# Performance work log

Hardware: AMD Instinct MI355X
Metric: run time of the kernel (lower is better)

## Reference

```python
import jax, jax.numpy as jnp
import numpy as np

K, d = 8, 8
D = K * d          # 64
B, T, N = 8, 12, 325


def _xavier(key, shape):
    fan_out, fan_in = shape
    lim = (6.0 / (fan_in + fan_out)) ** 0.5
    return jax.random.uniform(key, shape, jnp.float32, -lim, lim)


def setup_inputs() -> dict:
    key = jax.random.key(0)
    ks = jax.random.split(key, 8)
    return {
        "X": jax.random.normal(ks[0], (B, T, N, D), jnp.float32),
        "STE": jax.random.normal(ks[1], (B, T, N, D), jnp.float32),
        "adj": jax.random.randint(ks[2], (N, N), 0, 2, jnp.int32),
        "W7": _xavier(ks[3], (D, 2 * D)), "b7": jnp.zeros((D,), jnp.float32),
        "W8": _xavier(ks[4], (D, 2 * D)), "b8": jnp.zeros((D,), jnp.float32),
        "W9": _xavier(ks[5], (D, 2 * D)), "b9": jnp.zeros((D,), jnp.float32),
        "W10": _xavier(ks[6], (D, D)), "b10": jnp.zeros((D,), jnp.float32),
        "W11": _xavier(ks[7], (D, D)), "b11": jnp.zeros((D,), jnp.float32),
    }


def reference(X, STE, adj, W7, b7, W8, b8, W9, b9, W10, b10, W11, b11):
    # X, STE: [B, T, N, D]
    x = jnp.concatenate([X, STE], axis=-1)  # [B,T,N,2D]
    gelu = lambda t: jax.nn.gelu(t, approximate=False)  # torch F.gelu default = exact erf
    q = gelu(x @ W7.T + b7)  # [B,T,N,D]
    k = gelu(x @ W8.T + b8)
    v = gelu(x @ W9.T + b9)
    # split D into K heads of size d (equivalent to torch split(dim=-1)+cat(dim=0))
    heads = lambda t: t.reshape(B, T, N, K, d)
    q, k, v = heads(q), heads(k), heads(v)
    # scores: [K,B,T,N,N] == torch's [K*B,T,N,N]
    attn = jnp.einsum('btnkd,btmkd->kbtnm', q, k) / (d ** 0.5)
    attn = jnp.where(adj > 0, attn, jnp.float32(-9e15))
    attn = jax.nn.softmax(attn, axis=-1)
    out = jnp.einsum('kbtnm,btmkd->btnkd', attn, v).reshape(B, T, N, D)
    out = gelu(out @ W10.T + b10) @ W11.T + b11
    return out
```

## Files before the change

### kernel.cpp

```cpp
#include <hip/hip_runtime.h>
#include <math.h>

#define NN 325
#define BT 96
#define NROWS (BT * NN)
#define SCL (0.35355339059327373f * 1.4426950408889634f)

typedef _Float16 half_t;
typedef half_t half4_t __attribute__((ext_vector_type(4)));
typedef half_t half2_t __attribute__((ext_vector_type(2)));
typedef float float4_t __attribute__((ext_vector_type(4)));

__device__ __forceinline__ float gelu_f(float x) {
    return 0.5f * x * (1.0f + erff(x * 0.70710678118654752f));
}

__global__ void prep_kernel(const int* __restrict__ adj,
                            const float* __restrict__ W7,
                            const float* __restrict__ W8,
                            const float* __restrict__ W9,
                            const float* __restrict__ W10,
                            const float* __restrict__ W11,
                            unsigned int* __restrict__ packedT,
                            half_t* __restrict__ w789,
                            half_t* __restrict__ wab)
{
    int idx = blockIdx.x * 256 + threadIdx.x;
    if (idx < 11 * NN) {
        int w = idx / NN, n = idx - w * NN;
        unsigned int bits = 0u;
        #pragma unroll 8
        for (int j = 0; j < 32; ++j) {
            int m = w * 32 + j;
            if (m < NN && adj[n * NN + m] > 0) bits |= (1u << j);
        }
        packedT[w * NN + n] = bits;
    } else if (idx < 3575 + 24576) {
        int i = idx - 3575;
        int p = i >> 13, r = i & 8191;
        const float* Wp = (p == 0) ? W7 : (p == 1) ? W8 : W9;
        w789[i] = (half_t)Wp[r];
    } else if (idx < 3575 + 24576 + 8192) {
        int i = idx - 28151;
        int p = i >> 12, r = i & 4095;
        wab[i] = (half_t)(p ? W11[r] : W10[r]);
    }
}

#define XS 136

__device__ __forceinline__ void qkv_stage_w(const half_t* __restrict__ src,
                                            half_t* dst, int tid)
{
    #pragma unroll
    for (int idx = tid; idx < 1024; idx += 512) {
        int c = idx >> 4, g = idx & 15;
        *(uint4*)&dst[c * XS + g * 8] = *(const uint4*)&src[c * 128 + g * 8];
    }
}

__device__ __forceinline__ void qkv_compute(
    const half_t* x16, const half_t* wb, const float* __restrict__ b,
    half_t* __restrict__ outp, float oscale,
    int row0, int rbase, int ch, int l15, int quad)
{
    float4_t acc[2];
    #pragma unroll
    for (int cc = 0; cc < 2; ++cc) {
        float bias = b[(ch * 2 + cc) * 16 + l15];
        acc[cc] = (float4_t){bias, bias, bias, bias};
    }
    #pragma unroll
    for (int kk = 0; kk < 8; ++kk) {
        half4_t a = *(const half4_t*)&x16[(rbase + l15) * XS + kk * 16 + quad * 4];
        #pragma unroll
        for (int cc = 0; cc < 2; ++cc) {
            half4_t bf = *(const half4_t*)
                &wb[((ch * 2 + cc) * 16 + l15) * XS + kk * 16 + quad * 4];
            acc[cc] = __builtin_amdgcn_mfma_f32_16x16x16f16(a, bf, acc[cc], 0, 0, 0);
        }
    }
    #pragma unroll
    for (int cc = 0; cc < 2; ++cc) {
        #pragma unroll
        for (int rr = 0; rr < 4; ++rr) {
            int R = row0 + rbase + quad * 4 + rr;
            if (R < NROWS)
                outp[R * 64 + (ch * 2 + cc) * 16 + l15] =
                    (half_t)(gelu_f(acc[cc][rr]) * oscale);
        }
    }
}

__global__ __launch_bounds__(512) void qkv_kernel(
    const float* __restrict__ X, const float* __restrict__ STE,
    const half_t* __restrict__ w789,
    const float* __restrict__ b7, const float* __restrict__ b8,
    const float* __restrict__ b9,
    half_t* __restrict__ q, half_t* __restrict__ k, half_t* __restrict__ v)
{
    __shared__ __attribute__((aligned(16))) half_t x16[64 * XS];
    __shared__ __attribute__((aligned(16))) half_t wbuf[2][64 * XS];
    const int tid  = threadIdx.x;
    const int row0 = blockIdx.x * 64;

    #pragma unroll
    for (int idx = tid; idx < 2048; idx += 512) {
        int r = idx >> 5, c4 = idx & 31;
        int R = row0 + r;
        float4 f = {0.f, 0.f, 0.f, 0.f};
        if (R < NROWS)
            f = (c4 < 16) ? *(const float4*)(X + R * 64 + c4 * 4)
                          : *(const float4*)(STE + R * 64 + (c4 - 16) * 4);
        half4_t hv;
        hv[0] = (half_t)f.x; hv[1] = (half_t)f.y;
        hv[2] = (half_t)f.z; hv[3] = (half_t)f.w;
        *(half4_t*)&x16[r * XS + c4 * 4] = hv;
    }
    qkv_stage_w(w789, wbuf[0], tid);
    __syncthreads();

    const int lane = tid & 63, wv = tid >> 6;
    const int l15 = lane & 15, quad = lane >> 4;
    const int rbase = (wv & 3) * 16, ch = wv >> 2;

    qkv_stage_w(w789 + 8192, wbuf[1], tid);
    qkv_compute(x16, wbuf[0], b7, q, SCL, row0, rbase, ch, l15, quad);
    __syncthreads();

    qkv_stage_w(w789 + 16384, wbuf[0], tid);
    qkv_compute(x16, wbuf[1], b8, k, 1.0f, row0, rbase, ch, l15, quad);
    __syncthreads();

    qkv_compute(x16, wbuf[0], b9, v, 1.0f, row0, rbase, ch, l15, quad);
}

__global__ __launch_bounds__(256) void attn_kernel(
    const half_t* __restrict__ q16g, const half_t* __restrict__ k16g,
    const half_t* __restrict__ v16g, const unsigned int* __restrict__ packedT,
    half_t* __restrict__ ao)
{
    __shared__ __attribute__((aligned(16))) half_t K16[336 * 20];
    __shared__ __attribute__((aligned(16))) half_t VT16[16 * 344];
    const int tid = threadIdx.x;
    const int h = blockIdx.x, bt = blockIdx.y;
    const long base = (long)(bt * NN) * 64 + h * 8;

    const half4_t z4 = {(half_t)0.f, (half_t)0.f, (half_t)0.f, (half_t)0.f};

    for (int idx = tid; idx < 16 * 344 / 2; idx += 256)
        ((half2_t*)VT16)[idx] = (half2_t)(half_t)0.f;
    __syncthreads();
    for (int i = tid; i < 344; i += 256)
        VT16[8 * 344 + i] = (half_t)1.0f;

    for (int r = tid; r < 336; r += 256) {
        half4_t ka = z4, kb = z4;
        if (r < NN) {
            ka = *(const half4_t*)(k16g + base + r * 64);
            kb = *(const half4_t*)(k16g + base + r * 64 + 4);
        }
        *(half4_t*)&K16[r * 20]      = ka;
        *(half4_t*)&K16[r * 20 + 4]  = kb;
        *(half4_t*)&K16[r * 20 + 8]  = z4;
        *(half4_t*)&K16[r * 20 + 12] = z4;
    }

    for (int mp = tid; mp < 168; mp += 256) {
        int m0 = 2 * mp, m1 = 2 * mp + 1;
        half4_t v0a = z4, v0b = z4, v1a = z4, v1b = z4;
        if (m0 < NN) {
            v0a = *(const half4_t*)(v16g + base + m0 * 64);
            v0b = *(const half4_t*)(v16g + base + m0 * 64 + 4);
        }
        if (m1 < NN) {
            v1a = *(const half4_t*)(v16g + base + m1 * 64);
            v1b = *(const half4_t*)(v16g + base + m1 * 64 + 4);
        }
        #pragma unroll
        for (int c = 0; c < 4; ++c) {
            half2_t p0; p0[0] = v0a[c]; p0[1] = v1a[c];
            half2_t p1; p1[0] = v0b[c]; p1[1] = v1b[c];
            *(half2_t*)&VT16[c * 344 + 2 * mp]       = p0;
            *(half2_t*)&VT16[(c + 4) * 344 + 2 * mp] = p1;
        }
    }
    __syncthreads();

    const int lane = tid & 63;
    const int wv   = tid >> 6;
    const int l15  = lane & 15;
    const int quad = lane >> 4;
    const int qsh  = quad * 4;

    for (int t = wv; t < 21; t += 4) {
        const int n  = t * 16 + l15;
        const int nq = (n < NN) ? n : (NN - 1);

        half4_t qf = z4;
        if (quad < 2)
            qf = *(const half4_t*)(q16g + base + (long)nq * 64 + qsh);

        float rm = 0.0f;
        #pragma unroll
        for (int mt = 0; mt < 21; ++mt) {
            half4_t kf = *(const half4_t*)&K16[(mt * 16 + l15) * 20 + qsh];
            float4_t s = __builtin_amdgcn_mfma_f32_16x16x16f16(
                kf, qf, (float4_t){0.f, 0.f, 0.f, 0.f}, 0, 0, 0);
            rm = fmaxf(rm, fmaxf(fmaxf(s[0], s[1]), fmaxf(s[2], s[3])));
        }
        rm = fmaxf(rm, __shfl_xor(rm, 16, 64));
        rm = fmaxf(rm, __shfl_xor(rm, 32, 64));

        unsigned int mb[11];
        #pragma unroll
        for (int w = 0; w < 11; ++w) mb[w] = packedT[w * NN + nq];

        const float4_t cinit = {-rm, -rm, -rm, -rm};
        float4_t acc = {0.f, 0.f, 0.f, 0.f};
        #pragma unroll
        for (int mt = 0; mt < 21; ++mt) {
            half4_t kf = *(const half4_t*)&K16[(mt * 16 + l15) * 20 + qsh];
            float4_t s = __builtin_amdgcn_mfma_f32_16x16x16f16(
                kf, qf, cinit, 0, 0, 0);
            unsigned int sh = mb[mt >> 1] >> (((mt & 1) << 4) + qsh);
            float p0 = (sh & 1u) ? __builtin_amdgcn_exp2f(s[0]) : 0.f;
            float p1 = (sh & 2u) ? __builtin_amdgcn_exp2f(s[1]) : 0.f;
            float p2 = (sh & 4u) ? __builtin_amdgcn_exp2f(s[2]) : 0.f;
            float p3 = (sh & 8u) ? __builtin_amdgcn_exp2f(s[3]) : 0.f;
            half4_t pf;
            pf[0] = (half_t)p0; pf[1] = (half_t)p1;
            pf[2] = (half_t)p2; pf[3] = (half_t)p3;
            half4_t vf = *(const half4_t*)&VT16[l15 * 344 + mt * 16 + qsh];
            acc = __builtin_amdgcn_mfma_f32_16x16x16f16(vf, pf, acc, 0, 0, 0);
        }

        float sum = __shfl(acc[0], 32 + l15, 64);

        if (quad < 2 && n < NN) {
            float inv = 1.0f / sum;
            half4_t o;
            o[0] = (half_t)(acc[0] * inv); o[1] = (half_t)(acc[1] * inv);
            o[2] = (half_t)(acc[2] * inv); o[3] = (half_t)(acc[3] * inv);
            *(half4_t*)(ao + base + (long)n * 64 + qsh) = o;
        }
    }
}

#define PS 72

__global__ __launch_bounds__(512) void proj_kernel(
    const half_t* __restrict__ ao, const half_t* __restrict__ wab,
    const float* __restrict__ b10, const float* __restrict__ b11,
    float* __restrict__ out)
{
    __shared__ __attribute__((aligned(16))) half_t a16[64 * PS];
    __shared__ __attribute__((aligned(16))) half_t wA[64 * PS];
    __shared__ __attribute__((aligned(16))) half_t wB[64 * PS];
    __shared__ __attribute__((aligned(16))) half_t h16[64 * PS];
    const int tid  = threadIdx.x;
    const int row0 = blockIdx.x * 64;

    for (int idx = tid; idx < 512; idx += 512) {
        int r = idx >> 3, c8 = idx & 7;
        int R = row0 + r;
        uint4 u = {0u, 0u, 0u, 0u};
        if (R < NROWS) u = *(const uint4*)(ao + (long)R * 64 + c8 * 8);
        *(uint4*)&a16[r * PS + c8 * 8] = u;
        *(uint4*)&wA[r * PS + c8 * 8] = *(const uint4*)&wab[r * 64 + c8 * 8];
        *(uint4*)&wB[r * PS + c8 * 8] = *(const uint4*)&wab[4096 + r * 64 + c8 * 8];
    }
    __syncthreads();

    const int lane = tid & 63, wv = tid >> 6;
    const int l15 = lane & 15, quad = lane >> 4;
    const int rbase = (wv & 3) * 16, ch = wv >> 2;

    float4_t acc[2];
    #pragma unroll
    for (int cc = 0; cc < 2; ++cc) {
        float bias = b10[(ch * 2 + cc) * 16 + l15];
        acc[cc] = (float4_t){bias, bias, bias, bias};
    }
    #pragma unroll
    for (int kk = 0; kk < 4; ++kk) {
        half4_t a = *(const half4_t*)&a16[(rbase + l15) * PS + kk * 16 + quad * 4];
        #pragma unroll
        for (int cc = 0; cc < 2; ++cc) {
            half4_t bf = *(const half4_t*)
                &wA[((ch * 2 + cc) * 16 + l15) * PS + kk * 16 + quad * 4];
            acc[cc] = __builtin_amdgcn_mfma_f32_16x16x16f16(a, bf, acc[cc], 0, 0, 0);
        }
    }
    #pragma unroll
    for (int cc = 0; cc < 2; ++cc) {
        #pragma unroll
        for (int rr = 0; rr < 4; ++rr)
            h16[(rbase + quad * 4 + rr) * PS + (ch * 2 + cc) * 16 + l15] =
                (half_t)gelu_f(acc[cc][rr]);
    }
    __syncthreads();

    #pragma unroll
    for (int cc = 0; cc < 2; ++cc) {
        float bias = b11[(ch * 2 + cc) * 16 + l15];
        acc[cc] = (float4_t){bias, bias, bias, bias};
    }
    #pragma unroll
    for (int kk = 0; kk < 4; ++kk) {
        half4_t a = *(const half4_t*)&h16[(rbase + l15) * PS + kk * 16 + quad * 4];
        #pragma unroll
        for (int cc = 0; cc < 2; ++cc) {
            half4_t bf = *(const half4_t*)
                &wB[((ch * 2 + cc) * 16 + l15) * PS + kk * 16 + quad * 4];
            acc[cc] = __builtin_amdgcn_mfma_f32_16x16x16f16(a, bf, acc[cc], 0, 0, 0);
        }
    }
    #pragma unroll
    for (int cc = 0; cc < 2; ++cc) {
        #pragma unroll
        for (int rr = 0; rr < 4; ++rr) {
            int R = row0 + rbase + quad * 4 + rr;
            if (R < NROWS)
                out[R * 64 + (ch * 2 + cc) * 16 + l15] = acc[cc][rr];
        }
    }
}

extern "C" void kernel_launch(void* const* d_in, const int* in_sizes, int n_in,
                              void* d_out, int out_size, void* d_ws, size_t ws_size,
                              hipStream_t stream) {
    const float* X   = (const float*)d_in[0];
    const float* STE = (const float*)d_in[1];
    const int*   adj = (const int*)d_in[2];
    const float* W7  = (const float*)d_in[3];
    const float* b7  = (const float*)d_in[4];
    const float* W8  = (const float*)d_in[5];
    const float* b8  = (const float*)d_in[6];
    const float* W9  = (const float*)d_in[7];
    const float* b9  = (const float*)d_in[8];
    const float* W10 = (const float*)d_in[9];
    const float* b10 = (const float*)d_in[10];
    const float* W11 = (const float*)d_in[11];
    const float* b11 = (const float*)d_in[12];

    char* wsb = (char*)d_ws;
    const long S = (long)NROWS * 64;
    half_t* qb = (half_t*)wsb;
    half_t* kb = qb + S;
    half_t* vb = qb + 2 * S;
    half_t* ab = qb + 3 * S;
    unsigned int* pk = (unsigned int*)(wsb + 4 * S * sizeof(half_t));
    half_t* w789 = (half_t*)(wsb + 4 * S * sizeof(half_t) + 16384);
    half_t* wab  = w789 + 24576;

    prep_kernel<<<142, 256, 0, stream>>>(adj, W7, W8, W9, W10, W11,
                                         pk, w789, wab);
    qkv_kernel<<<dim3((NROWS + 63) / 64), 512, 0, stream>>>(
        X, STE, w789, b7, b8, b9, qb, kb, vb);
    attn_kernel<<<dim3(8, BT), 256, 0, stream>>>(qb, kb, vb, pk, ab);
    proj_kernel<<<dim3((NROWS + 63) / 64), 512, 0, stream>>>(
        ab, wab, b10, b11, (float*)d_out);
}
```

Baseline: 153.9 us.

## Fuse four stages into one persistent cooperative kernel with grid syncs

Replaces the four separate launches (prep, qkv, attention, projection) with a single cooperative persistent kernel whose blocks loop over work for each stage, separated by grid-wide syncs and a shared-memory union. The attention stage runs two head/bt units per 512-thread block, and adjacency-mask loads are hoisted ahead of the max pass. The aim is to remove launch gaps and inter-kernel tails, at the cost of a grid capped at 512 blocks, grid.sync overhead, and a larger register/LDS footprint that may limit occupancy. The old multi-kernel path is kept as a fallback if the cooperative launch fails.

Measured after the change: 393.0 us. 2.55x slower.

```diff
diff --git a/kernel.cpp b/kernel.cpp
--- a/kernel.cpp
+++ b/kernel.cpp
@@ -1,10 +1,15 @@
 #include <hip/hip_runtime.h>
+#include <hip/hip_cooperative_groups.h>
 #include <math.h>
+
+namespace cg = cooperative_groups;
 
 #define NN 325
 #define BT 96
 #define NROWS (BT * NN)
 #define SCL (0.35355339059327373f * 1.4426950408889634f)
+#define QKV_BLKS ((NROWS + 63) / 64)
+#define PREP_TOT (3575 + 24576 + 8192)
 
 typedef _Float16 half_t;
 typedef half_t half4_t __attribute__((ext_vector_type(4)));
@@ -13,6 +18,344 @@
 
 __device__ __forceinline__ float gelu_f(float x) {
     return 0.5f * x * (1.0f + erff(x * 0.70710678118654752f));
+}
+
+#define XS 136
+#define PS 72
+
+union __attribute__((aligned(16))) SMem {
+    struct { half_t x16[64 * XS]; half_t wbuf[2][64 * XS]; } qkv;
+    struct { half_t K16[2][336 * 20]; half_t VT16[2][16 * 344]; } attn;
+    struct {
+        half_t a16[64 * PS];
+        half_t wA[64 * PS];
+        half_t wB[64 * PS];
+        half_t h16[64 * PS];
+    } proj;
+};
+
+__device__ __forceinline__ void qkv_stage_w(const half_t* __restrict__ src,
+                                            half_t* dst, int tid)
+{
+    #pragma unroll
+    for (int idx = tid; idx < 1024; idx += 512) {
+        int c = idx >> 4, g = idx & 15;
+        *(uint4*)&dst[c * XS + g * 8] = *(const uint4*)&src[c * 128 + g * 8];
+    }
+}
+
+__device__ __forceinline__ void qkv_compute(
+    const half_t* x16, const half_t* wb, const float* __restrict__ b,
+    half_t* __restrict__ outp, float oscale,
+    int row0, int rbase, int ch, int l15, int quad)
+{
+    float4_t acc[2];
+    #pragma unroll
+    for (int cc = 0; cc < 2; ++cc) {
+        float bias = b[(ch * 2 + cc) * 16 + l15];
+        acc[cc] = (float4_t){bias, bias, bias, bias};
+    }
+    #pragma unroll
+    for (int kk = 0; kk < 8; ++kk) {
+        half4_t a = *(const half4_t*)&x16[(rbase + l15) * XS + kk * 16 + quad * 4];
+        #pragma unroll
+        for (int cc = 0; cc < 2; ++cc) {
+            half4_t bf = *(const half4_t*)
+                &wb[((ch * 2 + cc) * 16 + l15) * XS + kk * 16 + quad * 4];
+            acc[cc] = __builtin_amdgcn_mfma_f32_16x16x16f16(a, bf, acc[cc], 0, 0, 0);
+        }
+    }
+    #pragma unroll
+    for (int cc = 0; cc < 2; ++cc) {
+        #pragma unroll
+        for (int rr = 0; rr < 4; ++rr) {
+            int R = row0 + rbase + quad * 4 + rr;
+            if (R < NROWS)
+                outp[R * 64 + (ch * 2 + cc) * 16 + l15] =
+                    (half_t)(gelu_f(acc[cc][rr]) * oscale);
+        }
+    }
+}
+
+__device__ __forceinline__ void prep_work(
+    int idx, const int* __restrict__ adj,
+    const float* __restrict__ W7, const float* __restrict__ W8,
+    const float* __restrict__ W9, const float* __restrict__ W10,
+    const float* __restrict__ W11,
+    unsigned int* __restrict__ packedT,
+    half_t* __restrict__ w789, half_t* __restrict__ wab)
+{
+    if (idx < 11 * NN) {
+        int w = idx / NN, n = idx - w * NN;
+        unsigned int bits = 0u;
+        #pragma unroll 8
+        for (int j = 0; j < 32; ++j) {
+            int m = w * 32 + j;
+            if (m < NN && adj[n * NN + m] > 0) bits |= (1u << j);
+        }
+        packedT[w * NN + n] = bits;
+    } else if (idx < 3575 + 24576) {
+        int i = idx - 3575;
+        int p = i >> 13, r = i & 8191;
+        const float* Wp = (p == 0) ? W7 : (p == 1) ? W8 : W9;
+        w789[i] = (half_t)Wp[r];
+    } else if (idx < PREP_TOT) {
+        int i = idx - 28151;
+        int p = i >> 12, r = i & 4095;
+        wab[i] = (half_t)(p ? W11[r] : W10[r]);
+    }
+}
+
+__global__ __launch_bounds__(512, 4) void fused_kernel(
+    const float* __restrict__ X, const float* __restrict__ STE,
+    const int* __restrict__ adj,
+    const float* __restrict__ W7, const float* __restrict__ b7,
+    const float* __restrict__ W8, const float* __restrict__ b8,
+    const float* __restrict__ W9, const float* __restrict__ b9,
+    const float* __restrict__ W10, const float* __restrict__ b10,
+    const float* __restrict__ W11, const float* __restrict__ b11,
+    half_t* __restrict__ qb, half_t* __restrict__ kb, half_t* __restrict__ vb,
+    half_t* __restrict__ ab, unsigned int* __restrict__ pk,
+    half_t* __restrict__ w789, half_t* __restrict__ wab,
+    float* __restrict__ out)
+{
+    __shared__ SMem s;
+    cg::grid_group grid = cg::this_grid();
+    const int tid = threadIdx.x;
+    const int bx  = blockIdx.x;
+    const int nbx = gridDim.x;
+
+    for (int idx = bx * 512 + tid; idx < PREP_TOT; idx += nbx * 512)
+        prep_work(idx, adj, W7, W8, W9, W10, W11, pk, w789, wab);
+    __threadfence();
+    grid.sync();
+
+    for (int blk = bx; blk < QKV_BLKS; blk += nbx) {
+        half_t* x16 = s.qkv.x16;
+        const int row0 = blk * 64;
+
+        #pragma unroll
+        for (int idx = tid; idx < 2048; idx += 512) {
+            int r = idx >> 5, c4 = idx & 31;
+            int R = row0 + r;
+            float4 f = {0.f, 0.f, 0.f, 0.f};
+            if (R < NROWS)
+                f = (c4 < 16) ? *(const float4*)(X + R * 64 + c4 * 4)
+                              : *(const float4*)(STE + R * 64 + (c4 - 16) * 4);
+            half4_t hv;
+            hv[0] = (half_t)f.x; hv[1] = (half_t)f.y;
+            hv[2] = (half_t)f.z; hv[3] = (half_t)f.w;
+            *(half4_t*)&x16[r * XS + c4 * 4] = hv;
+        }
+        qkv_stage_w(w789, s.qkv.wbuf[0], tid);
+        __syncthreads();
+
+        const int lane = tid & 63, wv = tid >> 6;
+        const int l15 = lane & 15, quad = lane >> 4;
+        const int rbase = (wv & 3) * 16, ch = wv >> 2;
+
+        qkv_stage_w(w789 + 8192, s.qkv.wbuf[1], tid);
+        qkv_compute(x16, s.qkv.wbuf[0], b7, qb, SCL, row0, rbase, ch, l15, quad);
+        __syncthreads();
+
+        qkv_stage_w(w789 + 16384, s.qkv.wbuf[0], tid);
+        qkv_compute(x16, s.qkv.wbuf[1], b8, kb, 1.0f, row0, rbase, ch, l15, quad);
+        __syncthreads();
+
+        qkv_compute(x16, s.qkv.wbuf[0], b9, vb, 1.0f, row0, rbase, ch, l15, quad);
+        __syncthreads();
+    }
+    __threadfence();
+    grid.sync();
+
+    {
+        const int half_id = tid >> 8;
+        const int t2 = tid & 255;
+        for (int u2 = bx; u2 < (8 * BT) / 2; u2 += nbx) {
+            const int unit = u2 * 2 + half_id;
+            const int h = unit & 7, bt = unit >> 3;
+            const long base = (long)(bt * NN) * 64 + h * 8;
+            half_t* K16  = s.attn.K16[half_id];
+            half_t* VT16 = s.attn.VT16[half_id];
+
+            const half4_t z4 = {(half_t)0.f, (half_t)0.f, (half_t)0.f, (half_t)0.f};
+
+            for (int idx = t2; idx < 16 * 344 / 2; idx += 256)
+                ((half2_t*)VT16)[idx] = (half2_t)(half_t)0.f;
+            __syncthreads();
+            for (int i = t2; i < 344; i += 256)
+                VT16[8 * 344 + i] = (half_t)1.0f;
+
+            for (int r = t2; r < 336; r += 256) {
+                half4_t ka = z4, kbv = z4;
+                if (r < NN) {
+                    ka  = *(const half4_t*)(kb + base + r * 64);
+                    kbv = *(const half4_t*)(kb + base + r * 64 + 4);
+                }
+                *(half4_t*)&K16[r * 20]      = ka;
+                *(half4_t*)&K16[r * 20 + 4]  = kbv;
+                *(half4_t*)&K16[r * 20 + 8]  = z4;
+                *(half4_t*)&K16[r * 20 + 12] = z4;
+            }
+
+            for (int mp = t2; mp < 168; mp += 256) {
+                int m0 = 2 * mp, m1 = 2 * mp + 1;
+                half4_t v0a = z4, v0b = z4, v1a = z4, v1b = z4;
+                if (m0 < NN) {
+                    v0a = *(const half4_t*)(vb + base + m0 * 64);
+                    v0b = *(const half4_t*)(vb + base + m0 * 64 + 4);
+                }
+                if (m1 < NN) {
+                    v1a = *(const half4_t*)(vb + base + m1 * 64);
+                    v1b = *(const half4_t*)(vb + base + m1 * 64 + 4);
+                }
+                #pragma unroll
+                for (int c = 0; c < 4; ++c) {
+                    half2_t p0; p0[0] = v0a[c]; p0[1] = v1a[c];
+                    half2_t p1; p1[0] = v0b[c]; p1[1] = v1b[c];
+                    *(half2_t*)&VT16[c * 344 + 2 * mp]       = p0;
+                    *(half2_t*)&VT16[(c + 4) * 344 + 2 * mp] = p1;
+                }
+            }
+            __syncthreads();
+
+            const int lane = t2 & 63;
+            const int wv   = t2 >> 6;
+            const int l15  = lane & 15;
+            const int quad = lane >> 4;
+            const int qsh  = quad * 4;
+
+            for (int t = wv; t < 21; t += 4) {
+                const int n  = t * 16 + l15;
+                const int nq = (n < NN) ? n : (NN - 1);
+
+                half4_t qf = z4;
+                if (quad < 2)
+                    qf = *(const half4_t*)(qb + base + (long)nq * 64 + qsh);
+
+                unsigned int mb[11];
+                #pragma unroll
+                for (int w = 0; w < 11; ++w) mb[w] = pk[w * NN + nq];
+
+                float rm = 0.0f;
+                #pragma unroll
+                for (int mt = 0; mt < 21; ++mt) {
+                    half4_t kf = *(const half4_t*)&K16[(mt * 16 + l15) * 20 + qsh];
+                    float4_t sv = __builtin_amdgcn_mfma_f32_16x16x16f16(
+                        kf, qf, (float4_t){0.f, 0.f, 0.f, 0.f}, 0, 0, 0);
+                    rm = fmaxf(rm, fmaxf(fmaxf(sv[0], sv[1]), fmaxf(sv[2], sv[3])));
+                }
+                rm = fmaxf(rm, __shfl_xor(rm, 16, 64));
+                rm = fmaxf(rm, __shfl_xor(rm, 32, 64));
+
+                const float4_t cinit = {-rm, -rm, -rm, -rm};
+                float4_t acc = {0.f, 0.f, 0.f, 0.f};
+                #pragma unroll
+                for (int mt = 0; mt < 21; ++mt) {
+                    half4_t kf = *(const half4_t*)&K16[(mt * 16 + l15) * 20 + qsh];
+                    float4_t sv = __builtin_amdgcn_mfma_f32_16x16x16f16(
+                        kf, qf, cinit, 0, 0, 0);
+                    unsigned int sh = mb[mt >> 1] >> (((mt & 1) << 4) + qsh);
+                    float p0 = (sh & 1u) ? __builtin_amdgcn_exp2f(sv[0]) : 0.f;
+                    float p1 = (sh & 2u) ? __builtin_amdgcn_exp2f(sv[1]) : 0.f;
+                    float p2 = (sh & 4u) ? __builtin_amdgcn_exp2f(sv[2]) : 0.f;
+                    float p3 = (sh & 8u) ? __builtin_amdgcn_exp2f(sv[3]) : 0.f;
+                    half4_t pf;
+                    pf[0] = (half_t)p0; pf[1] = (half_t)p1;
+                    pf[2] = (half_t)p2; pf[3] = (half_t)p3;
+                    half4_t vf = *(const half4_t*)&VT16[l15 * 344 + mt * 16 + qsh];
+                    acc = __builtin_amdgcn_mfma_f32_16x16x16f16(vf, pf, acc, 0, 0, 0);
+                }
+
+                float sum = __shfl(acc[0], 32 + l15, 64);
+
+                if (quad < 2 && n < NN) {
+                    float inv = 1.0f / sum;
+                    half4_t o;
+                    o[0] = (half_t)(acc[0] * inv); o[1] = (half_t)(acc[1] * inv);
+                    o[2] = (half_t)(acc[2] * inv); o[3] = (half_t)(acc[3] * inv);
+                    *(half4_t*)(ab + base + (long)n * 64 + qsh) = o;
+                }
+            }
+            __syncthreads();
+        }
+    }
+    __threadfence();
+    grid.sync();
+
+    for (int blk = bx; blk < QKV_BLKS; blk += nbx) {
+        const int row0 = blk * 64;
+
+        for (int idx = tid; idx < 512; idx += 512) {
+            int r = idx >> 3, c8 = idx & 7;
+            int R = row0 + r;
+            uint4 u = {0u, 0u, 0u, 0u};
+            if (R < NROWS) u = *(const uint4*)(ab + (long)R * 64 + c8 * 8);
+            *(uint4*)&s.proj.a16[r * PS + c8 * 8] = u;
+            *(uint4*)&s.proj.wA[r * PS + c8 * 8] =
+                *(const uint4*)&wab[r * 64 + c8 * 8];
+            *(uint4*)&s.proj.wB[r * PS + c8 * 8] =
+                *(const uint4*)&wab[4096 + r * 64 + c8 * 8];
+        }
+        __syncthreads();
+
+        const int lane = tid & 63, wv = tid >> 6;
+        const int l15 = lane & 15, quad = lane >> 4;
+        const int rbase = (wv & 3) * 16, ch = wv >> 2;
+
+        float4_t acc[2];
+        #pragma unroll
+        for (int cc = 0; cc < 2; ++cc) {
+            float bias = b10[(ch * 2 + cc) * 16 + l15];
+            acc[cc] = (float4_t){bias, bias, bias, bias};
+        }
+        #pragma unroll
+        for (int kk = 0; kk < 4; ++kk) {
+            half4_t a = *(const half4_t*)
+                &s.proj.a16[(rbase + l15) * PS + kk * 16 + quad * 4];
+            #pragma unroll
+            for (int cc = 0; cc < 2; ++cc) {
+                half4_t bf = *(const half4_t*)
+                    &s.proj.wA[((ch * 2 + cc) * 16 + l15) * PS + kk * 16 + quad * 4];
+                acc[cc] = __builtin_amdgcn_mfma_f32_16x16x16f16(a, bf, acc[cc], 0, 0, 0);
+            }
+        }
+        #pragma unroll
+        for (int cc = 0; cc < 2; ++cc) {
+            #pragma unroll
+            for (int rr = 0; rr < 4; ++rr)
+                s.proj.h16[(rbase + quad * 4 + rr) * PS + (ch * 2 + cc) * 16 + l15] =
+                    (half_t)gelu_f(acc[cc][rr]);
+        }
+        __syncthreads();
+
+        #pragma unroll
+        for (int cc = 0; cc < 2; ++cc) {
+            float bias = b11[(ch * 2 + cc) * 16 + l15];
+            acc[cc] = (float4_t){bias, bias, bias, bias};
+        }
+        #pragma unroll
+        for (int kk = 0; kk < 4; ++kk) {
+            half4_t a = *(const half4_t*)
+                &s.proj.h16[(rbase + l15) * PS + kk * 16 + quad * 4];
+            #pragma unroll
+            for (int cc = 0; cc < 2; ++cc) {
+                half4_t bf = *(const half4_t*)
+                    &s.proj.wB[((ch * 2 + cc) * 16 + l15) * PS + kk * 16 + quad * 4];
+                acc[cc] = __builtin_amdgcn_mfma_f32_16x16x16f16(a, bf, acc[cc], 0, 0, 0);
+            }
+        }
+        #pragma unroll
+        for (int cc = 0; cc < 2; ++cc) {
+            #pragma unroll
+            for (int rr = 0; rr < 4; ++rr) {
+                int R = row0 + rbase + quad * 4 + rr;
+                if (R < NROWS)
+                    out[R * 64 + (ch * 2 + cc) * 16 + l15] = acc[cc][rr];
+            }
+        }
+        __syncthreads();
+    }
 }
 
 __global__ void prep_kernel(const int* __restrict__ adj,
@@ -26,70 +369,7 @@
                             half_t* __restrict__ wab)
 {
     int idx = blockIdx.x * 256 + threadIdx.x;
-    if (idx < 11 * NN) {
-        int w = idx / NN, n = idx - w * NN;
-        unsigned int bits = 0u;
-        #pragma unroll 8
-        for (int j = 0; j < 32; ++j) {
-            int m = w * 32 + j;
-            if (m < NN && adj[n * NN + m] > 0) bits |= (1u << j);
-        }
-        packedT[w * NN + n] = bits;
-    } else if (idx < 3575 + 24576) {
-        int i = idx - 3575;
-        int p = i >> 13, r = i & 8191;
-        const float* Wp = (p == 0) ? W7 : (p == 1) ? W8 : W9;
-        w789[i] = (half_t)Wp[r];
-    } else if (idx < 3575 + 24576 + 8192) {
-        int i = idx - 28151;
-        int p = i >> 12, r = i & 4095;
-        wab[i] = (half_t)(p ? W11[r] : W10[r]);
-    }
-}
-
-#define XS 136
-
-__device__ __forceinline__ void qkv_stage_w(const half_t* __restrict__ src,
-                                            half_t* dst, int tid)
-{
-    #pragma unroll
-    for (int idx = tid; idx < 1024; idx += 512) {
-        int c = idx >> 4, g = idx & 15;
-        *(uint4*)&dst[c * XS + g * 8] = *(const uint4*)&src[c * 128 + g * 8];
-    }
-}
-
-__device__ __forceinline__ void qkv_compute(
-    const half_t* x16, const half_t* wb, const float* __restrict__ b,
-    half_t* __restrict__ outp, float oscale,
-    int row0, int rbase, int ch, int l15, int quad)
-{
-    float4_t acc[2];
-    #pragma unroll
-    for (int cc = 0; cc < 2; ++cc) {
-        float bias = b[(ch * 2 + cc) * 16 + l15];
-        acc[cc] = (float4_t){bias, bias, bias, bias};
-    }
-    #pragma unroll
-    for (int kk = 0; kk < 8; ++kk) {
-        half4_t a = *(const half4_t*)&x16[(rbase + l15) * XS + kk * 16 + quad * 4];
-        #pragma unroll
-        for (int cc = 0; cc < 2; ++cc) {
-            half4_t bf = *(const half4_t*)
-                &wb[((ch * 2 + cc) * 16 + l15) * XS + kk * 16 + quad * 4];
-            acc[cc] = __builtin_amdgcn_mfma_f32_16x16x16f16(a, bf, acc[cc], 0, 0, 0);
-        }
-    }
-    #pragma unroll
-    for (int cc = 0; cc < 2; ++cc) {
-        #pragma unroll
-        for (int rr = 0; rr < 4; ++rr) {
-            int R = row0 + rbase + quad * 4 + rr;
-            if (R < NROWS)
-                outp[R * 64 + (ch * 2 + cc) * 16 + l15] =
-                    (half_t)(gelu_f(acc[cc][rr]) * oscale);
-        }
-    }
+    prep_work(idx, adj, W7, W8, W9, W10, W11, packedT, w789, wab);
 }
 
 __global__ __launch_bounds__(512) void qkv_kernel(
@@ -155,13 +435,13 @@
         VT16[8 * 344 + i] = (half_t)1.0f;
 
     for (int r = tid; r < 336; r += 256) {
-        half4_t ka = z4, kb = z4;
+        half4_t ka = z4, kbv = z4;
         if (r < NN) {
-            ka = *(const half4_t*)(k16g + base + r * 64);
-            kb = *(const half4_t*)(k16g + base + r * 64 + 4);
+            ka  = *(const half4_t*)(k16g + base + r * 64);
+            kbv = *(const half4_t*)(k16g + base + r * 64 + 4);
         }
         *(half4_t*)&K16[r * 20]      = ka;
-        *(half4_t*)&K16[r * 20 + 4]  = kb;
+        *(half4_t*)&K16[r * 20 + 4]  = kbv;
         *(half4_t*)&K16[r * 20 + 8]  = z4;
         *(half4_t*)&K16[r * 20 + 12] = z4;
     }
@@ -201,33 +481,33 @@
         if (quad < 2)
             qf = *(const half4_t*)(q16g + base + (long)nq * 64 + qsh);
 
+        unsigned int mb[11];
+        #pragma unroll
+        for (int w = 0; w < 11; ++w) mb[w] = packedT[w * NN + nq];
+
         float rm = 0.0f;
         #pragma unroll
         for (int mt = 0; mt < 21; ++mt) {
             half4_t kf = *(const half4_t*)&K16[(mt * 16 + l15) * 20 + qsh];
-            float4_t s = __builtin_amdgcn_mfma_f32_16x16x16f16(
+            float4_t sv = __builtin_amdgcn_mfma_f32_16x16x16f16(
                 kf, qf, (float4_t){0.f, 0.f, 0.f, 0.f}, 0, 0, 0);
-            rm = fmaxf(rm, fmaxf(fmaxf(s[0], s[1]), fmaxf(s[2], s[3])));
+            rm = fmaxf(rm, fmaxf(fmaxf(sv[0], sv[1]), fmaxf(sv[2], sv[3])));
         }
         rm = fmaxf(rm, __shfl_xor(rm, 16, 64));
         rm = fmaxf(rm, __shfl_xor(rm, 32, 64));
 
-        unsigned int mb[11];
-        #pragma unroll
-        for (int w = 0; w < 11; ++w) mb[w] = packedT[w * NN + nq];
-
         const float4_t cinit = {-rm, -rm, -rm, -rm};
         float4_t acc = {0.f, 0.f, 0.f, 0.f};
         #pragma unroll
         for (int mt = 0; mt < 21; ++mt) {
             half4_t kf = *(const half4_t*)&K16[(mt * 16 + l15) * 20 + qsh];
-            float4_t s = __builtin_amdgcn_mfma_f32_16x16x16f16(
+            float4_t sv = __builtin_amdgcn_mfma_f32_16x16x16f16(
                 kf, qf, cinit, 0, 0, 0);
             unsigned int sh = mb[mt >> 1] >> (((mt & 1) << 4) + qsh);
-            float p0 = (sh & 1u) ? __builtin_amdgcn_exp2f(s[0]) : 0.f;
-            float p1 = (sh & 2u) ? __builtin_amdgcn_exp2f(s[1]) : 0.f;
-            float p2 = (sh & 4u) ? __builtin_amdgcn_exp2f(s[2]) : 0.f;
-            float p3 = (sh & 8u) ? __builtin_amdgcn_exp2f(s[3]) : 0.f;
+            float p0 = (sh & 1u) ? __builtin_amdgcn_exp2f(sv[0]) : 0.f;
+            float p1 = (sh & 2u) ? __builtin_amdgcn_exp2f(sv[1]) : 0.f;
+            float p2 = (sh & 4u) ? __builtin_amdgcn_exp2f(sv[2]) : 0.f;
+            float p3 = (sh & 8u) ? __builtin_amdgcn_exp2f(sv[3]) : 0.f;
             half4_t pf;
             pf[0] = (half_t)p0; pf[1] = (half_t)p1;
             pf[2] = (half_t)p2; pf[3] = (half_t)p3;
@@ -246,8 +526,6 @@
         }
     }
 }
-
-#define PS 72
 
 __global__ __launch_bounds__(512) void proj_kernel(
     const half_t* __restrict__ ao, const half_t* __restrict__ wab,
@@ -343,6 +621,7 @@
     const float* b10 = (const float*)d_in[10];
     const float* W11 = (const float*)d_in[11];
     const float* b11 = (const float*)d_in[12];
+    float* outp = (float*)d_out;
 
     char* wsb = (char*)d_ws;
     const long S = (long)NROWS * 64;
@@ -354,6 +633,38 @@
     half_t* w789 = (half_t*)(wsb + 4 * S * sizeof(half_t) + 16384);
     half_t* wab  = w789 + 24576;
 
+    static int coop_grid = -2;
+    if (coop_grid == -2) {
+        int dev = 0;
+        (void)hipGetDevice(&dev);
+        int coopAttr = 0, numCU = 0, occ = 0;
+        (void)hipDeviceGetAttribute(&coopAttr,
+                                    hipDeviceAttributeCooperativeLaunch, dev);
+        (void)hipDeviceGetAttribute(&numCU,
+                                    hipDeviceAttributeMultiprocessorCount, dev);
+        hipError_t e = hipOccupancyMaxActiveBlocksPerMultiprocessor(
+            &occ, (const void*)fused_kernel, 512, 0);
+        long maxb = (long)occ * (long)numCU;
+        coop_grid = (e == hipSuccess && coopAttr && maxb >= 200)
+                        ? (int)(maxb < 512 ? maxb : 512) : 0;
+    }
+
+    if (coop_grid > 0) {
+        void* args[] = {
+            (void*)&X, (void*)&STE, (void*)&adj,
+            (void*)&W7, (void*)&b7, (void*)&W8, (void*)&b8,
+            (void*)&W9, (void*)&b9, (void*)&W10, (void*)&b10,
+            (void*)&W11, (void*)&b11,
+            (void*)&qb, (void*)&kb, (void*)&vb, (void*)&ab,
+            (void*)&pk, (void*)&w789, (void*)&wab, (void*)&outp
+        };
+        hipError_t err = hipLaunchCooperativeKernel(
+            (void*)fused_kernel, dim3(coop_grid), dim3(512), args, 0, stream);
+        if (err == hipSuccess) return;
+        (void)hipGetLastError();
+        coop_grid = 0;
+    }
+
     prep_kernel<<<142, 256, 0, stream>>>(adj, W7, W8, W9, W10, W11,
                                          pk, w789, wab);
     qkv_kernel<<<dim3((NROWS + 63) / 64), 512, 0, stream>>>(
```

## Fold prep kernel into qkv kernel and convert QKV weights in-kernel

Applied to the files above, without the earlier changes.

Removes the separate prep launch by appending extra blocks to the qkv grid that pack the adjacency bitmask and convert W10/W11 to fp16. The qkv blocks now read W7/W8/W9 directly as fp32 and convert to fp16 while staging into shared memory, which drops the fp16 weight copy in the workspace. The mask load in attention is also moved earlier to overlap with the max pass. The trade-off is redundant weight conversion in every qkv block and more fp32 weight traffic, in exchange for one fewer kernel launch and one fewer dependency step.

Result: faster. 148.6 us (-3.4%).

```diff
diff --git a/kernel.cpp b/kernel.cpp
--- a/kernel.cpp
+++ b/kernel.cpp
@@ -5,8 +5,13 @@
 #define BT 96
 #define NROWS (BT * NN)
 #define SCL (0.35355339059327373f * 1.4426950408889634f)
+#define QKV_BLKS ((NROWS + 63) / 64)
+#define PREP_ITEMS (11 * NN + 8192)
+#define PREP_BLKS ((PREP_ITEMS + 511) / 512)
+#define TOT_BLKS (QKV_BLKS + PREP_BLKS)
 
 typedef _Float16 half_t;
+typedef half_t half8_t __attribute__((ext_vector_type(8)));
 typedef half_t half4_t __attribute__((ext_vector_type(4)));
 typedef half_t half2_t __attribute__((ext_vector_type(2)));
 typedef float float4_t __attribute__((ext_vector_type(4)));
@@ -15,47 +20,23 @@
     return 0.5f * x * (1.0f + erff(x * 0.70710678118654752f));
 }
 
-__global__ void prep_kernel(const int* __restrict__ adj,
-                            const float* __restrict__ W7,
-                            const float* __restrict__ W8,
-                            const float* __restrict__ W9,
-                            const float* __restrict__ W10,
-                            const float* __restrict__ W11,
-                            unsigned int* __restrict__ packedT,
-                            half_t* __restrict__ w789,
-                            half_t* __restrict__ wab)
-{
-    int idx = blockIdx.x * 256 + threadIdx.x;
-    if (idx < 11 * NN) {
-        int w = idx / NN, n = idx - w * NN;
-        unsigned int bits = 0u;
-        #pragma unroll 8
-        for (int j = 0; j < 32; ++j) {
-            int m = w * 32 + j;
-            if (m < NN && adj[n * NN + m] > 0) bits |= (1u << j);
-        }
-        packedT[w * NN + n] = bits;
-    } else if (idx < 3575 + 24576) {
-        int i = idx - 3575;
-        int p = i >> 13, r = i & 8191;
-        const float* Wp = (p == 0) ? W7 : (p == 1) ? W8 : W9;
-        w789[i] = (half_t)Wp[r];
-    } else if (idx < 3575 + 24576 + 8192) {
-        int i = idx - 28151;
-        int p = i >> 12, r = i & 4095;
-        wab[i] = (half_t)(p ? W11[r] : W10[r]);
-    }
-}
-
 #define XS 136
-
-__device__ __forceinline__ void qkv_stage_w(const half_t* __restrict__ src,
-                                            half_t* dst, int tid)
+#define PS 72
+
+__device__ __forceinline__ void qkv_stage_wf(const float* __restrict__ src,
+                                             half_t* dst, int tid)
 {
     #pragma unroll
     for (int idx = tid; idx < 1024; idx += 512) {
         int c = idx >> 4, g = idx & 15;
-        *(uint4*)&dst[c * XS + g * 8] = *(const uint4*)&src[c * 128 + g * 8];
+        const float4* s4 = (const float4*)&src[c * 128 + g * 8];
+        float4 a = s4[0], b = s4[1];
+        half8_t h;
+        h[0] = (half_t)a.x; h[1] = (half_t)a.y;
+        h[2] = (half_t)a.z; h[3] = (half_t)a.w;
+        h[4] = (half_t)b.x; h[5] = (half_t)b.y;
+        h[6] = (half_t)b.z; h[7] = (half_t)b.w;
+        *(half8_t*)&dst[c * XS + g * 8] = h;
     }
 }
 
@@ -94,15 +75,39 @@
 
 __global__ __launch_bounds__(512) void qkv_kernel(
     const float* __restrict__ X, const float* __restrict__ STE,
-    const half_t* __restrict__ w789,
-    const float* __restrict__ b7, const float* __restrict__ b8,
-    const float* __restrict__ b9,
-    half_t* __restrict__ q, half_t* __restrict__ k, half_t* __restrict__ v)
-{
+    const int* __restrict__ adj,
+    const float* __restrict__ W7, const float* __restrict__ b7,
+    const float* __restrict__ W8, const float* __restrict__ b8,
+    const float* __restrict__ W9, const float* __restrict__ b9,
+    const float* __restrict__ W10, const float* __restrict__ W11,
+    half_t* __restrict__ q, half_t* __restrict__ k, half_t* __restrict__ v,
+    unsigned int* __restrict__ packedT, half_t* __restrict__ wab)
+{
+    const int tid = threadIdx.x;
+    const int bx  = blockIdx.x;
+
+    if (bx >= QKV_BLKS) {
+        int idx = (bx - QKV_BLKS) * 512 + tid;
+        if (idx < 11 * NN) {
+            int w = idx / NN, n = idx - w * NN;
+            unsigned int bits = 0u;
+            #pragma unroll 8
+            for (int j = 0; j < 32; ++j) {
+                int m = w * 32 + j;
+                if (m < NN && adj[n * NN + m] > 0) bits |= (1u << j);
+            }
+            packedT[w * NN + n] = bits;
+        } else if (idx < PREP_ITEMS) {
+            int i = idx - 11 * NN;
+            int p = i >> 12, r = i & 4095;
+            wab[i] = (half_t)(p ? W11[r] : W10[r]);
+        }
+        return;
+    }
+
     __shared__ __attribute__((aligned(16))) half_t x16[64 * XS];
     __shared__ __attribute__((aligned(16))) half_t wbuf[2][64 * XS];
-    const int tid  = threadIdx.x;
-    const int row0 = blockIdx.x * 64;
+    const int row0 = bx * 64;
 
     #pragma unroll
     for (int idx = tid; idx < 2048; idx += 512) {
@@ -117,18 +122,18 @@
         hv[2] = (half_t)f.z; hv[3] = (half_t)f.w;
         *(half4_t*)&x16[r * XS + c4 * 4] = hv;
     }
-    qkv_stage_w(w789, wbuf[0], tid);
+    qkv_stage_wf(W7, wbuf[0], tid);
     __syncthreads();
 
     const int lane = tid & 63, wv = tid >> 6;
     const int l15 = lane & 15, quad = lane >> 4;
     const int rbase = (wv & 3) * 16, ch = wv >> 2;
 
-    qkv_stage_w(w789 + 8192, wbuf[1], tid);
+    qkv_stage_wf(W8, wbuf[1], tid);
     qkv_compute(x16, wbuf[0], b7, q, SCL, row0, rbase, ch, l15, quad);
     __syncthreads();
 
-    qkv_stage_w(w789 + 16384, wbuf[0], tid);
+    qkv_stage_wf(W9, wbuf[0], tid);
     qkv_compute(x16, wbuf[1], b8, k, 1.0f, row0, rbase, ch, l15, quad);
     __syncthreads();
 
@@ -155,13 +160,13 @@
         VT16[8 * 344 + i] = (half_t)1.0f;
 
     for (int r = tid; r < 336; r += 256) {
-        half4_t ka = z4, kb = z4;
+        half4_t ka = z4, kbv = z4;
         if (r < NN) {
-            ka = *(const half4_t*)(k16g + base + r * 64);
-            kb = *(const half4_t*)(k16g + base + r * 64 + 4);
+            ka  = *(const half4_t*)(k16g + base + r * 64);
+            kbv = *(const half4_t*)(k16g + base + r * 64 + 4);
         }
         *(half4_t*)&K16[r * 20]      = ka;
-        *(half4_t*)&K16[r * 20 + 4]  = kb;
+        *(half4_t*)&K16[r * 20 + 4]  = kbv;
         *(half4_t*)&K16[r * 20 + 8]  = z4;
         *(half4_t*)&K16[r * 20 + 12] = z4;
     }
@@ -201,33 +206,33 @@
         if (quad < 2)
             qf = *(const half4_t*)(q16g + base + (long)nq * 64 + qsh);
 
+        unsigned int mb[11];
+        #pragma unroll
+        for (int w = 0; w < 11; ++w) mb[w] = packedT[w * NN + nq];
+
         float rm = 0.0f;
         #pragma unroll
         for (int mt = 0; mt < 21; ++mt) {
             half4_t kf = *(const half4_t*)&K16[(mt * 16 + l15) * 20 + qsh];
-            float4_t s = __builtin_amdgcn_mfma_f32_16x16x16f16(
+            float4_t sv = __builtin_amdgcn_mfma_f32_16x16x16f16(
                 kf, qf, (float4_t){0.f, 0.f, 0.f, 0.f}, 0, 0, 0);
-            rm = fmaxf(rm, fmaxf(fmaxf(s[0], s[1]), fmaxf(s[2], s[3])));
+            rm = fmaxf(rm, fmaxf(fmaxf(sv[0], sv[1]), fmaxf(sv[2], sv[3])));
         }
         rm = fmaxf(rm, __shfl_xor(rm, 16, 64));
         rm = fmaxf(rm, __shfl_xor(rm, 32, 64));
 
-        unsigned int mb[11];
-        #pragma unroll
-        for (int w = 0; w < 11; ++w) mb[w] = packedT[w * NN + nq];
-
         const float4_t cinit = {-rm, -rm, -rm, -rm};
         float4_t acc = {0.f, 0.f, 0.f, 0.f};
         #pragma unroll
         for (int mt = 0; mt < 21; ++mt) {
             half4_t kf = *(const half4_t*)&K16[(mt * 16 + l15) * 20 + qsh];
-            float4_t s = __builtin_amdgcn_mfma_f32_16x16x16f16(
+            float4_t sv = __builtin_amdgcn_mfma_f32_16x16x16f16(
                 kf, qf, cinit, 0, 0, 0);
             unsigned int sh = mb[mt >> 1] >> (((mt & 1) << 4) + qsh);
-            float p0 = (sh & 1u) ? __builtin_amdgcn_exp2f(s[0]) : 0.f;
-            float p1 = (sh & 2u) ? __builtin_amdgcn_exp2f(s[1]) : 0.f;
-            float p2 = (sh & 4u) ? __builtin_amdgcn_exp2f(s[2]) : 0.f;
-            float p3 = (sh & 8u) ? __builtin_amdgcn_exp2f(s[3]) : 0.f;
+            float p0 = (sh & 1u) ? __builtin_amdgcn_exp2f(sv[0]) : 0.f;
+            float p1 = (sh & 2u) ? __builtin_amdgcn_exp2f(sv[1]) : 0.f;
+            float p2 = (sh & 4u) ? __builtin_amdgcn_exp2f(sv[2]) : 0.f;
+            float p3 = (sh & 8u) ? __builtin_amdgcn_exp2f(sv[3]) : 0.f;
             half4_t pf;
             pf[0] = (half_t)p0; pf[1] = (half_t)p1;
             pf[2] = (half_t)p2; pf[3] = (half_t)p3;
@@ -246,8 +251,6 @@
         }
     }
 }
-
-#define PS 72
 
 __global__ __launch_bounds__(512) void proj_kernel(
     const half_t* __restrict__ ao, const half_t* __restrict__ wab,
@@ -351,13 +354,11 @@
     half_t* vb = qb + 2 * S;
     half_t* ab = qb + 3 * S;
     unsigned int* pk = (unsigned int*)(wsb + 4 * S * sizeof(half_t));
-    half_t* w789 = (half_t*)(wsb + 4 * S * sizeof(half_t) + 16384);
-    half_t* wab  = w789 + 24576;
-
-    prep_kernel<<<142, 256, 0, stream>>>(adj, W7, W8, W9, W10, W11,
-                                         pk, w789, wab);
-    qkv_kernel<<<dim3((NROWS + 63) / 64), 512, 0, stream>>>(
-        X, STE, w789, b7, b8, b9, qb, kb, vb);
+    half_t* wab = (half_t*)(wsb + 4 * S * sizeof(half_t) + 16384);
+
+    qkv_kernel<<<dim3(TOT_BLKS), 512, 0, stream>>>(
+        X, STE, adj, W7, b7, W8, b8, W9, b9, W10, W11,
+        qb, kb, vb, pk, wab);
     attn_kernel<<<dim3(8, BT), 256, 0, stream>>>(qb, kb, vb, pk, ab);
     proj_kernel<<<dim3((NROWS + 63) / 64), 512, 0, stream>>>(
         ab, wab, b10, b11, (float*)d_out);
```
